# Kernel optimization log

Hardware: AMD Instinct MI355X
Metric: run time of the kernel (lower is better)

Reference implementation:

```python
import jax, jax.numpy as jnp
import numpy as np

NUM_HEADS = 4
KERNEL = 7
DILATION = 1
EMBED = 128
CTX = 256
RANK = 8
HEAD_DIM = EMBED // NUM_HEADS
SCALE = HEAD_DIM ** (-0.5)


def setup_inputs() -> dict:
    key = jax.random.key(0)
    ks = jax.random.split(key, 16)
    B, H, W = 4, 64, 64
    inp = {
        "x": jax.random.normal(ks[0], (B, H, W, EMBED), jnp.float32),
        "context": jax.random.normal(ks[1], (B, CTX), jnp.float32),
        # base QKV linear (torch Linear: y = x @ W.T + b)
        "Wqkv": jax.random.normal(ks[2], (3 * EMBED, EMBED), jnp.float32) * 0.02,
        "bqkv": jax.random.normal(ks[3], (3 * EMBED,), jnp.float32) * 0.02,
        # bilinear LoRA params (init scale 0.01 as in source)
        "A": jax.random.normal(ks[4], (EMBED, RANK), jnp.float32) * 0.01,
        "Blora": jax.random.normal(ks[5], (CTX, RANK), jnp.float32) * 0.01,
        "Vlora": jax.random.normal(ks[6], (3 * EMBED, RANK), jnp.float32) * 0.01,
        # gate MLP: Linear(ctx,16) -> ReLU -> Linear(16,1) -> Sigmoid
        "g1w": jax.random.normal(ks[7], (16, CTX), jnp.float32) * 0.05,
        "g1b": jnp.zeros((16,), jnp.float32),
        "g2w": jnp.full((1, 16), -5.0, jnp.float32) * 0.0 + jax.random.normal(ks[8], (1, 16), jnp.float32) * 0.01 - 5.0 / 16.0,
        "g2b": jnp.full((1,), -5.0, jnp.float32),
        # output projection
        "Wproj": jax.random.normal(ks[9], (EMBED, EMBED), jnp.float32) * 0.02,
        "bproj": jnp.zeros((EMBED,), jnp.float32),
    }
    return inp


def _windows(t, H, W):
    # t: [B, nh, H+2p, W+2p, d] -> [B, nh, H, W, K^2, d]
    ws = []
    for i in range(KERNEL):
        for j in range(KERNEL):
            ws.append(t[:, :, i * DILATION:i * DILATION + H, j * DILATION:j * DILATION + W, :])
    return jnp.stack(ws, axis=4)


def reference(x, context, Wqkv, bqkv, A, Blora, Vlora, g1w, g1b, g2w, g2b, Wproj, bproj):
    B, H, W, C = x.shape
    nh, hd = NUM_HEADS, HEAD_DIM
    # context-modulated QKV: base + alpha * ((xA) * (cB)) V^T
    base = x @ Wqkv.T + bqkv                                   # [B,H,W,3C]
    c_proj = context @ Blora                                   # [B,r]
    delta = ((x @ A) * c_proj[:, None, None, :]) @ Vlora.T     # [B,H,W,3C]
    alpha = jax.nn.sigmoid(jax.nn.relu(context @ g1w.T + g1b) @ g2w.T + g2b)  # [B,1]
    qkv = base + alpha[:, None, None, :] * delta               # [B,H,W,3C]

    qkv = qkv.reshape(B, H, W, 3, nh, hd)
    qkv = jnp.transpose(qkv, (3, 0, 4, 1, 2, 5))               # [3,B,nh,H,W,hd]
    q, k, v = qkv[0], qkv[1], qkv[2]

    pad = DILATION * (KERNEL - 1) // 2
    pw = ((0, 0), (0, 0), (pad, pad), (pad, pad), (0, 0))
    k_p = jnp.pad(k, pw)
    v_p = jnp.pad(v, pw)
    kw = _windows(k_p, H, W)                                   # [B,nh,H,W,K2,hd]
    vw = _windows(v_p, H, W)

    attn = jnp.einsum('bnijd,bnijkd->bnijk', q, kw) * SCALE    # [B,nh,H,W,K2]
    attn = jax.nn.softmax(attn, axis=-1)
    out = jnp.einsum('bnijk,bnijkd->bnijd', attn, vw)          # [B,nh,H,W,hd]

    out = jnp.transpose(out, (0, 2, 3, 1, 4)).reshape(B, H, W, C)
    out = out @ Wproj.T + bproj
    return out
```

## Files before the change

### kernel.cpp

```cpp
#include <hip/hip_runtime.h>
#include <cstddef>

#define CTXDIM 256
#define RANK 8
#define KW 7
#define SCALE 0.17677669529663687f
#define NPIX 16384
#define PLANE16 (NPIX * 128)
#define WSTRIDE 136

typedef _Float16 half8 __attribute__((ext_vector_type(8)));
typedef _Float16 half2_t __attribute__((ext_vector_type(2)));
typedef float floatx4 __attribute__((ext_vector_type(4)));
typedef float floatx16 __attribute__((ext_vector_type(16)));
typedef int intx4 __attribute__((ext_vector_type(4)));

struct Params {
  const float *x, *ctx, *Wqkv, *bqkv, *A, *Blora, *Vlora;
  const float *g1w, *g1b, *g2w, *g2b, *Wproj, *bproj;
  float* out;
  _Float16* qkv16;
  _Float16* at16;
};

__device__ __forceinline__ void compute_cal(const Params& p, int tid,
                                            float* cal_s) {
  const int b = tid >> 6, lane = tid & 63;
  const float c0 = p.ctx[b * CTXDIM + lane];
  const float c1 = p.ctx[b * CTXDIM + 64 + lane];
  const float c2 = p.ctx[b * CTXDIM + 128 + lane];
  const float c3 = p.ctx[b * CTXDIM + 192 + lane];
  float cp[RANK];
#pragma unroll
  for (int r = 0; r < RANK; ++r) {
    float q = c0 * p.Blora[lane * RANK + r] + c1 * p.Blora[(64 + lane) * RANK + r] +
              c2 * p.Blora[(128 + lane) * RANK + r] + c3 * p.Blora[(192 + lane) * RANK + r];
#pragma unroll
    for (int s = 32; s; s >>= 1) q += __shfl_xor(q, s, 64);
    cp[r] = q;
  }
  float gacc = 0.f;
#pragma unroll
  for (int h = 0; h < 16; ++h) {
    float q = c0 * p.g1w[h * CTXDIM + lane] + c1 * p.g1w[h * CTXDIM + 64 + lane] +
              c2 * p.g1w[h * CTXDIM + 128 + lane] + c3 * p.g1w[h * CTXDIM + 192 + lane];
#pragma unroll
    for (int s = 32; s; s >>= 1) q += __shfl_xor(q, s, 64);
    gacc += fmaxf(q + p.g1b[h], 0.f) * p.g2w[h];
  }
  if (lane == 0) {
    const float alpha = 1.f / (1.f + __expf(-(gacc + p.g2b[0])));
#pragma unroll
    for (int r = 0; r < RANK; ++r) cal_s[b * RANK + r] = alpha * cp[r];
  }
}

__device__ __forceinline__ void stage_rows_f16(const float* __restrict__ src,
                                               _Float16* dst, int tid) {
  const int row = tid >> 2;
  const int c0 = (tid & 3) * 32;
  const float* sp = src + (size_t)row * 128 + c0;
  _Float16* dp = dst + row * WSTRIDE + c0;
#pragma unroll
  for (int i = 0; i < 4; ++i) {
    const float4 a = *(const float4*)(sp + i * 8);
    const float4 b = *(const float4*)(sp + i * 8 + 4);
    half8 o;
    o[0] = (_Float16)a.x; o[1] = (_Float16)a.y;
    o[2] = (_Float16)a.z; o[3] = (_Float16)a.w;
    o[4] = (_Float16)b.x; o[5] = (_Float16)b.y;
    o[6] = (_Float16)b.z; o[7] = (_Float16)b.w;
    *(half8*)(dp + i * 8) = o;
  }
}

__global__ __launch_bounds__(256) void gemm1_kernel(Params p) {
  __shared__ __align__(16) _Float16 xs[64 * WSTRIDE];
  __shared__ __align__(16) _Float16 wsh[64 * WSTRIDE];
  __shared__ float cal_s[32];
  const int tid = threadIdx.x;
  const int bx = blockIdx.x, byg = blockIdx.y, z = blockIdx.z;
  const int m0 = z * 4096 + bx * 64;

  compute_cal(p, tid, cal_s);
  stage_rows_f16(p.x + (size_t)m0 * 128, xs, tid);
  __syncthreads();

  const int lane = tid & 63;
  const int w = tid >> 6;
  const int r = lane & 15;
  const int quad = lane >> 4;
  const int k = tid & 127;
  const int hgrp = tid >> 7;
  const float4 a0 = *(const float4*)&p.A[k * RANK];
  const float4 a1 = *(const float4*)&p.A[k * RANK + 4];
  const float* cb = &cal_s[z * RANK];
  const float c0 = cb[0], c1 = cb[1], c2 = cb[2], c3 = cb[3];
  const float c4 = cb[4], c5 = cb[5], c6 = cb[6], c7 = cb[7];

  for (int i = 0; i < 3; ++i) {
    const int n0 = (byg * 3 + i) * 64;

#pragma unroll
    for (int rr = 0; rr < 32; ++rr) {
      const int row = hgrp * 32 + rr;
      const int o = n0 + row;
      const float4 v0 = *(const float4*)&p.Vlora[o * RANK];
      const float4 v1 = *(const float4*)&p.Vlora[o * RANK + 4];
      float d = a0.x * v0.x * c0;
      d = fmaf(a0.y * v0.y, c1, d);
      d = fmaf(a0.z * v0.z, c2, d);
      d = fmaf(a0.w * v0.w, c3, d);
      d = fmaf(a1.x * v1.x, c4, d);
      d = fmaf(a1.y * v1.y, c5, d);
      d = fmaf(a1.z * v1.z, c6, d);
      d = fmaf(a1.w * v1.w, c7, d);
      wsh[row * WSTRIDE + k] = (_Float16)(p.Wqkv[o * 128 + k] + d);
    }
    __syncthreads();

    const _Float16* ap = xs + (w * 16 + r) * WSTRIDE + quad * 8;
    const _Float16* bp = wsh + r * WSTRIDE + quad * 8;
    floatx4 acc0 = {0.f, 0.f, 0.f, 0.f};
    floatx4 acc1 = acc0, acc2 = acc0, acc3 = acc0;
#pragma unroll
    for (int kc = 0; kc < 4; ++kc) {
      const half8 a  = *(const half8*)(ap + kc * 32);
      const half8 b0 = *(const half8*)(bp + kc * 32);
      const half8 b1 = *(const half8*)(bp + 16 * WSTRIDE + kc * 32);
      const half8 b2 = *(const half8*)(bp + 32 * WSTRIDE + kc * 32);
      const half8 b3 = *(const half8*)(bp + 48 * WSTRIDE + kc * 32);
      acc0 = __builtin_amdgcn_mfma_f32_16x16x32_f16(a, b0, acc0, 0, 0, 0);
      acc1 = __builtin_amdgcn_mfma_f32_16x16x32_f16(a, b1, acc1, 0, 0, 0);
      acc2 = __builtin_amdgcn_mfma_f32_16x16x32_f16(a, b2, acc2, 0, 0, 0);
      acc3 = __builtin_amdgcn_mfma_f32_16x16x32_f16(a, b3, acc3, 0, 0, 0);
    }

    const int mbase = m0 + w * 16 + quad * 4;
    floatx4 accs[4] = {acc0, acc1, acc2, acc3};
#pragma unroll
    for (int nt = 0; nt < 4; ++nt) {
      const int ncol = n0 + nt * 16 + r;
      const float bv = p.bqkv[ncol];
      _Float16* cp = p.qkv16 + (size_t)(ncol >> 7) * PLANE16 +
                     (size_t)mbase * 128 + (ncol & 127);
#pragma unroll
      for (int reg = 0; reg < 4; ++reg)
        cp[(size_t)reg * 128] = (_Float16)(accs[nt][reg] + bv);
    }
    if (i != 2) __syncthreads();
  }
}

__device__ __forceinline__ int vta(int d, int k) {
  const int sig = (d + (d >> 3)) & 7;
  return d * 256 + (((k >> 3) ^ sig) << 3) + (k & 7);
}

__device__ __forceinline__ int packh(float x, float y) {
  half2_t h;
  h[0] = (_Float16)x;
  h[1] = (_Float16)y;
  return __builtin_bit_cast(int, h);
}

template <int MT0, int W>
__device__ __forceinline__ void attn_wave(const Params& p,
                                          const _Float16* kls,
                                          const _Float16* vtl,
                                          half8 qb0, half8 qb1,
                                          int m31, int l5, int pi, int pj,
                                          int b, int ti, int tj, int h) {
  const floatx16 zz = {0.f,0.f,0.f,0.f,0.f,0.f,0.f,0.f,
                       0.f,0.f,0.f,0.f,0.f,0.f,0.f,0.f};
  floatx16 acc[5];
#pragma unroll
  for (int mt = 0; mt < 5; ++mt) {
    const int Mt = MT0 + mt;
    const half8 ka0 = *(const half8*)&kls[(Mt * 32 + m31) * 40 + l5 * 8];
    const half8 ka1 = *(const half8*)&kls[(Mt * 32 + m31) * 40 + 16 + l5 * 8];
    floatx16 a = zz;
    a = __builtin_amdgcn_mfma_f32_32x32x16_f16(ka0, qb0, a, 0, 0, 0);
    a = __builtin_amdgcn_mfma_f32_32x32x16_f16(ka1, qb1, a, 0, 0, 0);
    acc[mt] = a;
  }

  bool vR[14];
#pragma unroll
  for (int i = 0; i < 14; ++i) vR[i] = (unsigned)(i - pi) < 7u;
  bool vC[8];
#pragma unroll
  for (int c8 = 0; c8 < 8; ++c8) {
    const int hcv = (c8 & 3) + 8 * (c8 >> 2) + 4 * l5;
    vC[c8] = (unsigned)(hcv - pj) < 7u;
  }

  float mxp[4] = {-1e30f, -1e30f, -1e30f, -1e30f};
#pragma unroll
  for (int mt = 0; mt < 5; ++mt) {
#pragma unroll
    for (int reg = 0; reg < 16; ++reg) {
      const bool v = vR[2 * (MT0 + mt) + (reg >> 3)] &&
                     vC[(reg & 3) + 4 * ((reg >> 2) & 1)];
      const float x = v ? acc[mt][reg] : -1e30f;
      acc[mt][reg] = x;
      mxp[reg & 3] = fmaxf(mxp[reg & 3], x);
    }
  }
  float mx = fmaxf(fmaxf(mxp[0], mxp[1]), fmaxf(mxp[2], mxp[3]));
  mx = fmaxf(mx, __shfl_xor(mx, 32, 64));

  const float SC2 = SCALE * 1.4426950408889634f;
  float sp[4] = {0.f, 0.f, 0.f, 0.f};
#pragma unroll
  for (int mt = 0; mt < 5; ++mt) {
#pragma unroll
    for (int reg = 0; reg < 16; ++reg) {
      const float pv = exp2f((acc[mt][reg] - mx) * SC2);
      acc[mt][reg] = pv;
      sp[reg & 3] += pv;
    }
  }
  float sum = (sp[0] + sp[1]) + (sp[2] + sp[3]);
  sum += __shfl_xor(sum, 32, 64);
  const float inv = 1.f / sum;

  floatx16 oacc = zz;
  const int sigd = (m31 + (m31 >> 3)) & 7;
  const int vbase = m31 * 256;
#pragma unroll
  for (int kk = 0; kk < 10; ++kk) {
    const int ks = MT0 * 2 + kk;
    const int mt = (ks >> 1) - MT0;
    const int r8 = 8 * (ks & 1);
    const int E00 = packh(acc[mt][r8 + 0] * inv, acc[mt][r8 + 1] * inv);
    const int E01 = packh(acc[mt][r8 + 2] * inv, acc[mt][r8 + 3] * inv);
    const int E10 = packh(acc[mt][r8 + 4] * inv, acc[mt][r8 + 5] * inv);
    const int E11 = packh(acc[mt][r8 + 6] * inv, acc[mt][r8 + 7] * inv);
    const int R00 = __shfl_xor(E00, 32, 64);
    const int R01 = __shfl_xor(E01, 32, 64);
    const int R10 = __shfl_xor(E10, 32, 64);
    const int R11 = __shfl_xor(E11, 32, 64);
    const int A0 = l5 ? R10 : E00;
    const int A1 = l5 ? R11 : E01;
    const int A2 = l5 ? E10 : R00;
    const int A3 = l5 ? E11 : R01;
    const intx4 ai = {A0, A1, A2, A3};
    const half8 af = __builtin_bit_cast(half8, ai);
    const half8 vb = *(const half8*)&vtl[vbase + (((2 * ks + l5) ^ sigd) << 3)];
    oacc = __builtin_amdgcn_mfma_f32_32x32x16_f16(af, vb, oacc, 0, 0, 0);
  }

#pragma unroll
  for (int reg = 0; reg < 16; ++reg) {
    const int rowM = (reg & 3) + 8 * (reg >> 2) + 4 * l5;
    const int pxt = W * 32 + rowM;
    const int n = b * 4096 + (ti * 8 + (pxt >> 3)) * 64 + tj * 8 + (pxt & 7);
    p.at16[(size_t)n * 128 + h * 32 + m31] = (_Float16)oacc[reg];
  }
}

__global__ __launch_bounds__(128, 2) void attn_kernel(Params p) {
  __shared__ __align__(16) _Float16 kls[224 * 40];
  __shared__ __align__(16) _Float16 vtl[32 * 256];

  const int bid = blockIdx.x;
  const int h  = bid & 3;
  const int tj = (bid >> 2) & 7;
  const int ti = (bid >> 5) & 7;
  const int b  = bid >> 8;
  const int tid = threadIdx.x;
  const int lane = tid & 63;
  const int w = tid >> 6;
  const int m31 = lane & 31;
  const int l5 = lane >> 5;

  const _Float16* kpl = p.qkv16 + PLANE16;
  const _Float16* vpl = p.qkv16 + 2 * (size_t)PLANE16;

  const int pix = w * 32 + m31;
  const int pi = pix >> 3, pj = pix & 7;
  const int nq = b * 4096 + (ti * 8 + pi) * 64 + tj * 8 + pj;
  const half8 qb0 = *(const half8*)(p.qkv16 + (size_t)nq * 128 + h * 32 + l5 * 8);
  const half8 qb1 = *(const half8*)(p.qkv16 + (size_t)nq * 128 + h * 32 + 16 + l5 * 8);

  for (int idx = tid; idx < 896; idx += 128) {
    const int d = idx & 31;
    const int kk = idx >> 5;
    const int k = (kk >> 1) * 16 + 14 + (kk & 1);
    vtl[vta(d, k)] = (_Float16)0.f;
  }

  const int i0 = ti * 8 - 3;
  const int j0 = tj * 8 - 3;
  for (int s = tid; s < 784; s += 128) {
    const int pp = s >> 2;
    const int d8 = (s & 3) * 8;
    const int hr = pp / 14;
    const int hc = pp - hr * 14;
    const int row = hr * 16 + hc;
    const int ii = i0 + hr;
    const int jj = j0 + hc;
    half8 kv = {0, 0, 0, 0, 0, 0, 0, 0};
    half8 vv = {0, 0, 0, 0, 0, 0, 0, 0};
    if ((unsigned)ii < 64u && (unsigned)jj < 64u) {
      const size_t g = (size_t)(b * 4096 + ii * 64 + jj) * 128 + h * 32 + d8;
      kv = *(const half8*)(kpl + g);
      vv = *(const half8*)(vpl + g);
    }
    *(half8*)&kls[row * 40 + d8] = kv;
#pragma unroll
    for (int e = 0; e < 8; ++e)
      vtl[vta(d8 + e, row)] = vv[e];
  }
  __syncthreads();

  if (w == 0)
    attn_wave<0, 0>(p, kls, vtl, qb0, qb1, m31, l5, pi, pj, b, ti, tj, h);
  else
    attn_wave<2, 1>(p, kls, vtl, qb0, qb1, m31, l5, pi, pj, b, ti, tj, h);
}

__global__ __launch_bounds__(256) void gemm2_kernel(Params p) {
  __shared__ __align__(16) _Float16 wsh[64 * WSTRIDE];
  const int tid = threadIdx.x;
  const int m0 = blockIdx.x * 64;
  const int n0 = blockIdx.y * 64;

  stage_rows_f16(p.Wproj + (size_t)n0 * 128, wsh, tid);
  __syncthreads();

  const int lane = tid & 63;
  const int w = tid >> 6;
  const int r = lane & 15;
  const int quad = lane >> 4;
  const _Float16* ap = p.at16 + (size_t)(m0 + w * 16 + r) * 128 + quad * 8;
  const _Float16* bp = wsh + r * WSTRIDE + quad * 8;

  floatx4 acc0 = {0.f, 0.f, 0.f, 0.f};
  floatx4 acc1 = acc0, acc2 = acc0, acc3 = acc0;
#pragma unroll
  for (int kc = 0; kc < 4; ++kc) {
    const half8 a  = *(const half8*)(ap + kc * 32);
    const half8 b0 = *(const half8*)(bp + kc * 32);
    const half8 b1 = *(const half8*)(bp + 16 * WSTRIDE + kc * 32);
    const half8 b2 = *(const half8*)(bp + 32 * WSTRIDE + kc * 32);
    const half8 b3 = *(const half8*)(bp + 48 * WSTRIDE + kc * 32);
    acc0 = __builtin_amdgcn_mfma_f32_16x16x32_f16(a, b0, acc0, 0, 0, 0);
    acc1 = __builtin_amdgcn_mfma_f32_16x16x32_f16(a, b1, acc1, 0, 0, 0);
    acc2 = __builtin_amdgcn_mfma_f32_16x16x32_f16(a, b2, acc2, 0, 0, 0);
    acc3 = __builtin_amdgcn_mfma_f32_16x16x32_f16(a, b3, acc3, 0, 0, 0);
  }

  const int mbase = m0 + w * 16 + quad * 4;
  floatx4 accs[4] = {acc0, acc1, acc2, acc3};
#pragma unroll
  for (int nt = 0; nt < 4; ++nt) {
    const int n = n0 + nt * 16 + r;
    const float bv = p.bproj[n];
    float* cp = p.out + (size_t)mbase * 128 + n;
#pragma unroll
    for (int reg = 0; reg < 4; ++reg)
      cp[(size_t)reg * 128] = accs[nt][reg] + bv;
  }
}

extern "C" void kernel_launch(void* const* d_in, const int* in_sizes, int n_in,
                              void* d_out, int out_size, void* d_ws, size_t ws_size,
                              hipStream_t stream) {
  char* ws = (char*)d_ws;
  Params hp;
  hp.x     = (const float*)d_in[0];
  hp.ctx   = (const float*)d_in[1];
  hp.Wqkv  = (const float*)d_in[2];
  hp.bqkv  = (const float*)d_in[3];
  hp.A     = (const float*)d_in[4];
  hp.Blora = (const float*)d_in[5];
  hp.Vlora = (const float*)d_in[6];
  hp.g1w   = (const float*)d_in[7];
  hp.g1b   = (const float*)d_in[8];
  hp.g2w   = (const float*)d_in[9];
  hp.g2b   = (const float*)d_in[10];
  hp.Wproj = (const float*)d_in[11];
  hp.bproj = (const float*)d_in[12];
  hp.out   = (float*)d_out;
  hp.qkv16 = (_Float16*)(ws + (1u << 20));
  hp.at16  = (_Float16*)(ws + (14u << 20));

  gemm1_kernel<<<dim3(64, 2, 4), 256, 0, stream>>>(hp);
  attn_kernel<<<1024, 128, 0, stream>>>(hp);
  gemm2_kernel<<<dim3(256, 2), 256, 0, stream>>>(hp);
}
```

Measured before the change: 50.24 us.

## Fuse neighborhood attention with output projection in one kernel

```diff
diff --git a/kernel.cpp b/kernel.cpp
--- a/kernel.cpp
+++ b/kernel.cpp
@@ -8,6 +8,10 @@
 #define NPIX 16384
 #define PLANE16 (NPIX * 128)
 #define WSTRIDE 136
+
+#define KHEAD 8960
+#define VHEAD 8192
+#define VBASE (4 * KHEAD)
 
 typedef _Float16 half8 __attribute__((ext_vector_type(8)));
 typedef _Float16 half2_t __attribute__((ext_vector_type(2)));
@@ -164,13 +168,11 @@
   return __builtin_bit_cast(int, h);
 }
 
-template <int MT0, int W>
-__device__ __forceinline__ void attn_wave(const Params& p,
-                                          const _Float16* kls,
-                                          const _Float16* vtl,
-                                          half8 qb0, half8 qb1,
-                                          int m31, int l5, int pi, int pj,
-                                          int b, int ti, int tj, int h) {
+template <int MT0>
+__device__ __forceinline__ floatx16 attn_wave(const _Float16* kls,
+                                              const _Float16* vtl,
+                                              half8 qb0, half8 qb1,
+                                              int m31, int l5, int pi, int pj) {
   const floatx16 zz = {0.f,0.f,0.f,0.f,0.f,0.f,0.f,0.f,
                        0.f,0.f,0.f,0.f,0.f,0.f,0.f,0.f};
   floatx16 acc[5];
@@ -250,41 +252,38 @@
     const half8 vb = *(const half8*)&vtl[vbase + (((2 * ks + l5) ^ sigd) << 3)];
     oacc = __builtin_amdgcn_mfma_f32_32x32x16_f16(af, vb, oacc, 0, 0, 0);
   }
-
-#pragma unroll
-  for (int reg = 0; reg < 16; ++reg) {
-    const int rowM = (reg & 3) + 8 * (reg >> 2) + 4 * l5;
-    const int pxt = W * 32 + rowM;
-    const int n = b * 4096 + (ti * 8 + (pxt >> 3)) * 64 + tj * 8 + (pxt & 7);
-    p.at16[(size_t)n * 128 + h * 32 + m31] = (_Float16)oacc[reg];
-  }
-}
-
-__global__ __launch_bounds__(128, 2) void attn_kernel(Params p) {
-  __shared__ __align__(16) _Float16 kls[224 * 40];
-  __shared__ __align__(16) _Float16 vtl[32 * 256];
+  return oacc;
+}
+
+__global__ __launch_bounds__(256, 1) void attn_proj_kernel(Params p) {
+  __shared__ __align__(16) _Float16 sm[4 * KHEAD + 4 * VHEAD];
 
   const int bid = blockIdx.x;
-  const int h  = bid & 3;
-  const int tj = (bid >> 2) & 7;
-  const int ti = (bid >> 5) & 7;
-  const int b  = bid >> 8;
+  const int tj = bid & 7;
+  const int ti = (bid >> 3) & 7;
+  const int b  = bid >> 6;
   const int tid = threadIdx.x;
+  const int h = tid >> 6;
   const int lane = tid & 63;
-  const int w = tid >> 6;
   const int m31 = lane & 31;
   const int l5 = lane >> 5;
 
+  _Float16* kls = sm + h * KHEAD;
+  _Float16* vtl = sm + VBASE + h * VHEAD;
+
   const _Float16* kpl = p.qkv16 + PLANE16;
   const _Float16* vpl = p.qkv16 + 2 * (size_t)PLANE16;
 
-  const int pix = w * 32 + m31;
-  const int pi = pix >> 3, pj = pix & 7;
-  const int nq = b * 4096 + (ti * 8 + pi) * 64 + tj * 8 + pj;
-  const half8 qb0 = *(const half8*)(p.qkv16 + (size_t)nq * 128 + h * 32 + l5 * 8);
-  const half8 qb1 = *(const half8*)(p.qkv16 + (size_t)nq * 128 + h * 32 + 16 + l5 * 8);
-
-  for (int idx = tid; idx < 896; idx += 128) {
+  const int pi0 = m31 >> 3, pj0 = m31 & 7;
+  const int pi1 = 4 + pi0, pj1 = pj0;
+  const int nq0 = b * 4096 + (ti * 8 + pi0) * 64 + tj * 8 + pj0;
+  const int nq1 = nq0 + 4 * 64;
+  const half8 q00 = *(const half8*)(p.qkv16 + (size_t)nq0 * 128 + h * 32 + l5 * 8);
+  const half8 q01 = *(const half8*)(p.qkv16 + (size_t)nq0 * 128 + h * 32 + 16 + l5 * 8);
+  const half8 q10 = *(const half8*)(p.qkv16 + (size_t)nq1 * 128 + h * 32 + l5 * 8);
+  const half8 q11 = *(const half8*)(p.qkv16 + (size_t)nq1 * 128 + h * 32 + 16 + l5 * 8);
+
+  for (int idx = lane; idx < 896; idx += 64) {
     const int d = idx & 31;
     const int kk = idx >> 5;
     const int k = (kk >> 1) * 16 + 14 + (kk & 1);
@@ -293,7 +292,7 @@
 
   const int i0 = ti * 8 - 3;
   const int j0 = tj * 8 - 3;
-  for (int s = tid; s < 784; s += 128) {
+  for (int s = lane; s < 784; s += 64) {
     const int pp = s >> 2;
     const int d8 = (s & 3) * 8;
     const int hr = pp / 14;
@@ -315,53 +314,50 @@
   }
   __syncthreads();
 
-  if (w == 0)
-    attn_wave<0, 0>(p, kls, vtl, qb0, qb1, m31, l5, pi, pj, b, ti, tj, h);
-  else
-    attn_wave<2, 1>(p, kls, vtl, qb0, qb1, m31, l5, pi, pj, b, ti, tj, h);
-}
-
-__global__ __launch_bounds__(256) void gemm2_kernel(Params p) {
-  __shared__ __align__(16) _Float16 wsh[64 * WSTRIDE];
-  const int tid = threadIdx.x;
-  const int m0 = blockIdx.x * 64;
-  const int n0 = blockIdx.y * 64;
-
-  stage_rows_f16(p.Wproj + (size_t)n0 * 128, wsh, tid);
+  const floatx16 o0 = attn_wave<0>(kls, vtl, q00, q01, m31, l5, pi0, pj0);
+  const floatx16 o1 = attn_wave<2>(kls, vtl, q10, q11, m31, l5, pi1, pj1);
   __syncthreads();
 
-  const int lane = tid & 63;
-  const int w = tid >> 6;
+  _Float16* at_s = sm;
+#pragma unroll
+  for (int reg = 0; reg < 16; ++reg) {
+    const int rowM = (reg & 3) + 8 * (reg >> 2) + 4 * l5;
+    at_s[rowM * WSTRIDE + h * 32 + m31] = (_Float16)o0[reg];
+    at_s[(32 + rowM) * WSTRIDE + h * 32 + m31] = (_Float16)o1[reg];
+  }
+  _Float16* wsh = sm + VBASE;
+  stage_rows_f16(p.Wproj, wsh, tid);
+  stage_rows_f16(p.Wproj + 64 * 128, wsh + 64 * WSTRIDE, tid);
+  __syncthreads();
+
   const int r = lane & 15;
   const int quad = lane >> 4;
-  const _Float16* ap = p.at16 + (size_t)(m0 + w * 16 + r) * 128 + quad * 8;
+  const _Float16* ap = at_s + (h * 16 + r) * WSTRIDE + quad * 8;
   const _Float16* bp = wsh + r * WSTRIDE + quad * 8;
-
-  floatx4 acc0 = {0.f, 0.f, 0.f, 0.f};
-  floatx4 acc1 = acc0, acc2 = acc0, acc3 = acc0;
+  floatx4 acc[8];
+#pragma unroll
+  for (int nt = 0; nt < 8; ++nt) acc[nt] = (floatx4){0.f, 0.f, 0.f, 0.f};
 #pragma unroll
   for (int kc = 0; kc < 4; ++kc) {
-    const half8 a  = *(const half8*)(ap + kc * 32);
-    const half8 b0 = *(const half8*)(bp + kc * 32);
-    const half8 b1 = *(const half8*)(bp + 16 * WSTRIDE + kc * 32);
-    const half8 b2 = *(const half8*)(bp + 32 * WSTRIDE + kc * 32);
-    const half8 b3 = *(const half8*)(bp + 48 * WSTRIDE + kc * 32);
-    acc0 = __builtin_amdgcn_mfma_f32_16x16x32_f16(a, b0, acc0, 0, 0, 0);
-    acc1 = __builtin_amdgcn_mfma_f32_16x16x32_f16(a, b1, acc1, 0, 0, 0);
-    acc2 = __builtin_amdgcn_mfma_f32_16x16x32_f16(a, b2, acc2, 0, 0, 0);
-    acc3 = __builtin_amdgcn_mfma_f32_16x16x32_f16(a, b3, acc3, 0, 0, 0);
-  }
-
-  const int mbase = m0 + w * 16 + quad * 4;
-  floatx4 accs[4] = {acc0, acc1, acc2, acc3};
-#pragma unroll
-  for (int nt = 0; nt < 4; ++nt) {
-    const int n = n0 + nt * 16 + r;
-    const float bv = p.bproj[n];
-    float* cp = p.out + (size_t)mbase * 128 + n;
-#pragma unroll
-    for (int reg = 0; reg < 4; ++reg)
-      cp[(size_t)reg * 128] = accs[nt][reg] + bv;
+    const half8 a = *(const half8*)(ap + kc * 32);
+#pragma unroll
+    for (int nt = 0; nt < 8; ++nt) {
+      const half8 bf = *(const half8*)(bp + nt * 16 * WSTRIDE + kc * 32);
+      acc[nt] = __builtin_amdgcn_mfma_f32_16x16x32_f16(a, bf, acc[nt], 0, 0, 0);
+    }
+  }
+
+  const int rbase = b * 4096 + (ti * 8 + h * 2 + (quad >> 1)) * 64 +
+                    tj * 8 + (quad & 1) * 4;
+  float bv[8];
+#pragma unroll
+  for (int nt = 0; nt < 8; ++nt) bv[nt] = p.bproj[nt * 16 + r];
+#pragma unroll
+  for (int reg = 0; reg < 4; ++reg) {
+    float* cp = p.out + (size_t)(rbase + reg) * 128;
+#pragma unroll
+    for (int nt = 0; nt < 8; ++nt)
+      cp[nt * 16 + r] = acc[nt][reg] + bv[nt];
   }
 }
 
@@ -388,6 +384,5 @@
   hp.at16  = (_Float16*)(ws + (14u << 20));
 
   gemm1_kernel<<<dim3(64, 2, 4), 256, 0, stream>>>(hp);
-  attn_kernel<<<1024, 128, 0, stream>>>(hp);
-  gemm2_kernel<<<dim3(256, 2), 256, 0, stream>>>(hp);
-}
+  attn_proj_kernel<<<256, 256, 0, stream>>>(hp);
+}
```

Measured after the change: 49.30 us. Within noise of the previous version (-1.9%).
